# Optimization experiments

Hardware: AMD Instinct MI355X
Metric: run time of the kernel (lower is better)

## Reference

```python
import jax, jax.numpy as jnp
import numpy as np

NU, NM, E, L = 100000, 20000, 3200000, 1000000
FD, H = 128, 64


def setup_inputs() -> dict:
    key = jax.random.key(0)
    ks = jax.random.split(key, 32)
    s = 0.05
    inp = {
        'movie_x': jax.random.normal(ks[0], (NM, FD), jnp.float32),
        'edge_src_user': jax.random.randint(ks[1], (E,), 0, NU),
        'edge_dst_movie': jax.random.randint(ks[2], (E,), 0, NM),
        'label_user': jax.random.randint(ks[3], (L,), 0, NU),
        'label_movie': jax.random.randint(ks[4], (L,), 0, NM),
        'user_emb': jax.random.normal(ks[5], (NU, H), jnp.float32) * s,
        'proj_w': jax.random.normal(ks[6], (FD, H), jnp.float32) * s,
        'proj_b': jnp.zeros((H,), jnp.float32),
        'dec_w1': jax.random.normal(ks[7], (2 * H, H), jnp.float32) * s,
        'dec_b1': jnp.zeros((H,), jnp.float32),
        'dec_w2': jax.random.normal(ks[8], (H, 1), jnp.float32) * s,
        'dec_b2': jnp.zeros((1,), jnp.float32),
    }
    i = 9
    for layer in ('1', '2'):
        for rel in ('um', 'mu'):
            inp[f'w{layer}_{rel}_l'] = jax.random.normal(ks[i], (H, H), jnp.float32) * s; i += 1
            inp[f'b{layer}_{rel}_l'] = jnp.zeros((H,), jnp.float32)
            inp[f'w{layer}_{rel}_r'] = jax.random.normal(ks[i], (H, H), jnp.float32) * s; i += 1
    return inp


def _sage(x_src, x_dst, e_src, e_dst, n_dst, w_l, b_l, w_r):
    # PyG SAGEConv, aggr='mean': out = lin_l(mean_j x_src[j]) + lin_r(x_dst)
    msg = x_src[e_src]                                      # [E, H] gather
    agg = jax.ops.segment_sum(msg, e_dst, num_segments=n_dst)
    cnt = jax.ops.segment_sum(jnp.ones((e_dst.shape[0],), x_src.dtype), e_dst, num_segments=n_dst)
    agg = agg / jnp.maximum(cnt, 1.0)[:, None]
    return agg @ w_l + b_l + x_dst @ w_r


def reference(movie_x, edge_src_user, edge_dst_movie, label_user, label_movie,
              user_emb, proj_w, proj_b,
              w1_um_l, b1_um_l, w1_um_r, w1_mu_l, b1_mu_l, w1_mu_r,
              w2_um_l, b2_um_l, w2_um_r, w2_mu_l, b2_mu_l, w2_mu_r,
              dec_w1, dec_b1, dec_w2, dec_b2):
    nu, nm = user_emb.shape[0], movie_x.shape[0]
    user0 = user_emb
    movie0 = movie_x @ proj_w + proj_b
    # conv1 (user->movie and movie->user), then ReLU
    movie1 = jax.nn.relu(_sage(user0, movie0, edge_src_user, edge_dst_movie, nm, w1_um_l, b1_um_l, w1_um_r))
    user1 = jax.nn.relu(_sage(movie0, user0, edge_dst_movie, edge_src_user, nu, w1_mu_l, b1_mu_l, w1_mu_r))
    # conv2 (no activation)
    movie2 = _sage(user1, movie1, edge_src_user, edge_dst_movie, nm, w2_um_l, b2_um_l, w2_um_r)
    user2 = _sage(movie1, user1, edge_dst_movie, edge_src_user, nu, w2_mu_l, b2_mu_l, w2_mu_r)
    # edge decoder: gather -> concat -> MLP
    x = jnp.concatenate([user2[label_user], movie2[label_movie]], axis=-1)  # [L, 2H]
    x = jax.nn.relu(x @ dec_w1 + dec_b1)
    return x @ dec_w2 + dec_b2
```

## Files before the change

### kernel.cpp

```cpp
#include <hip/hip_runtime.h>

static constexpr int NU = 100000;
static constexpr int NM = 20000;
static constexpr int NE = 3200000;
static constexpr int NL = 1000000;
static constexpr int FD = 128;
static constexpr int H  = 64;

static constexpr int MBK = 16;
static constexpr int UBK = 64;
static constexpr int NBM = NM / MBK;
static constexpr int NBU = (NU + UBK - 1) / UBK;
static constexpr int CAP_M = 4096;
static constexpr int CAP_U = 3072;
static constexpr int B3C = 16384;

typedef __attribute__((ext_vector_type(8))) short short8v;
typedef __attribute__((ext_vector_type(4))) float f32x4;

__device__ __forceinline__ ushort bf16rne(float x) {
  unsigned u = __float_as_uint(x);
  return (ushort)((u + 0x7fffu + ((u >> 16) & 1u)) >> 16);
}

__global__ void k_binit2(int* __restrict__ bcur_m, int* __restrict__ bcur_u) {
  int i = blockIdx.x * 256 + threadIdx.x;
  if (i < NBM) bcur_m[i] = i * CAP_M;
  if (i < NBU) bcur_u[i] = i * CAP_U;
}

__global__ void __launch_bounds__(256) k_bin3(
    const int* __restrict__ esrc, const int* __restrict__ edst,
    int* __restrict__ bcur_m, int* __restrict__ bcur_u,
    unsigned* __restrict__ pairs_m, unsigned* __restrict__ pairs_u, int nbPerSide) {
  __shared__ int cnt[NBU];
  __shared__ int base[NBU];
  int tid = threadIdx.x;
  bool um = (int)blockIdx.x < nbPerSide;
  int cb = um ? blockIdx.x : blockIdx.x - nbPerSide;
  int nbs = um ? NBM : NBU;
  int sh = um ? 4 : 6;
  int* bcur = um ? bcur_m : bcur_u;
  unsigned* pairs = um ? pairs_m : pairs_u;
  const int* keys = um ? edst : esrc;
  const int* vals = um ? esrc : edst;
  int e0 = cb * B3C, e1 = min(e0 + B3C, NE);
  for (int i = tid; i < nbs; i += 256) cnt[i] = 0;
  __syncthreads();
  for (int e = e0 + (tid << 2); e < e1; e += 1024) {
    int4 k = *(const int4*)(keys + e);
    atomicAdd(&cnt[k.x >> sh], 1);
    atomicAdd(&cnt[k.y >> sh], 1);
    atomicAdd(&cnt[k.z >> sh], 1);
    atomicAdd(&cnt[k.w >> sh], 1);
  }
  __syncthreads();
  for (int i = tid; i < nbs; i += 256) {
    int c = cnt[i];
    if (c > 0) base[i] = atomicAdd(&bcur[i], c);
    cnt[i] = 0;
  }
  __syncthreads();
  int lsh = um ? 17 : 15;
  unsigned lmask = um ? 15u : 63u;
  for (int e = e0 + (tid << 2); e < e1; e += 1024) {
    int4 k = *(const int4*)(keys + e);
    int4 v = *(const int4*)(vals + e);
    int ks[4] = {k.x, k.y, k.z, k.w};
    int vs[4] = {v.x, v.y, v.z, v.w};
    #pragma unroll
    for (int j = 0; j < 4; ++j) {
      int b = ks[j] >> sh;
      int r = atomicAdd(&cnt[b], 1);
      pairs[base[b] + r] = (((unsigned)ks[j] & lmask) << lsh) | (unsigned)vs[j];
    }
  }
}

__global__ void __launch_bounds__(256) k_sortb4(
    const unsigned* __restrict__ pairs_m, const unsigned* __restrict__ pairs_u,
    const int* __restrict__ bcur_m, const int* __restrict__ bcur_u,
    int* __restrict__ st_m, int* __restrict__ dg_m, int* __restrict__ out_m,
    int* __restrict__ st_u, int* __restrict__ dg_u, ushort* __restrict__ out_u) {
  __shared__ int cnt[64];
  __shared__ int cbase[64];
  const unsigned* pairs; const int* bcur; int* start; int* deg;
  int b, npb, shift, cap, n; unsigned mask;
  bool um = (int)blockIdx.x < NBM;
  if (um) {
    pairs = pairs_m; bcur = bcur_m; start = st_m; deg = dg_m;
    b = blockIdx.x; npb = MBK; shift = 17; mask = 0x1FFFFu; cap = CAP_M; n = NM;
  } else {
    pairs = pairs_u; bcur = bcur_u; start = st_u; deg = dg_u;
    b = blockIdx.x - NBM; npb = UBK; shift = 15; mask = 0x7FFFu; cap = CAP_U; n = NU;
  }
  int tid = threadIdx.x;
  if (tid < 64) cnt[tid] = 0;
  __syncthreads();
  int e0 = b * cap, e1 = bcur[b];
  for (int e = e0 + tid; e < e1; e += 256) atomicAdd(&cnt[pairs[e] >> shift], 1);
  __syncthreads();
  if (tid < 64) {
    int c = cnt[tid];
    int v = c;
    #pragma unroll
    for (int off = 1; off < 64; off <<= 1) {
      int t = __shfl_up(v, off, 64);
      if (tid >= off) v += t;
    }
    int basee = e0 + v - c;
    cbase[tid] = basee;
    int node = b * npb + tid;
    if (tid < npb && node < n) { start[node] = basee; deg[node] = c; }
    cnt[tid] = 0;
  }
  __syncthreads();
  for (int e = e0 + tid; e < e1; e += 256) {
    unsigned v = pairs[e];
    int loc = (int)(v >> shift);
    int r = atomicAdd(&cnt[loc], 1);
    if (um) out_m[cbase[loc] + r] = (int)(v & mask);
    else    out_u[cbase[loc] + r] = (ushort)(v & mask);
  }
}

#define ACC4(vv)                                                           \
  a0 += __uint_as_float((vv).x << 16); a1 += __uint_as_float((vv).x & 0xffff0000u); \
  a2 += __uint_as_float((vv).y << 16); a3 += __uint_as_float((vv).y & 0xffff0000u); \
  a4 += __uint_as_float((vv).z << 16); a5 += __uint_as_float((vv).z & 0xffff0000u); \
  a6 += __uint_as_float((vv).w << 16); a7 += __uint_as_float((vv).w & 0xffff0000u);

__device__ __forceinline__ void agg_node_w8(const ushort* __restrict__ feat,
                                            const int* __restrict__ idxs,
                                            int s, int degn, float* __restrict__ out,
                                            int d, int lane) {
  int f8 = lane & 7, p = lane >> 3;
  int e = s + degn;
  float a0 = 0.f, a1 = 0.f, a2 = 0.f, a3 = 0.f, a4 = 0.f, a5 = 0.f, a6 = 0.f, a7 = 0.f;
  int i = s;
  for (; i + 32 <= e; i += 32) {
    int s0 = idxs[i + 0 + p];
    int s1 = idxs[i + 8 + p];
    int s2 = idxs[i + 16 + p];
    int s3 = idxs[i + 24 + p];
    uint4 v0 = *(const uint4*)(feat + ((size_t)s0 << 6) + (f8 << 3));
    uint4 v1 = *(const uint4*)(feat + ((size_t)s1 << 6) + (f8 << 3));
    uint4 v2 = *(const uint4*)(feat + ((size_t)s2 << 6) + (f8 << 3));
    uint4 v3 = *(const uint4*)(feat + ((size_t)s3 << 6) + (f8 << 3));
    ACC4(v0) ACC4(v1) ACC4(v2) ACC4(v3)
  }
  for (; i < e; i += 8) {
    int ii = i + p;
    bool ok = ii < e;
    int sj = idxs[ok ? ii : i];
    uint4 v = *(const uint4*)(feat + ((size_t)sj << 6) + (f8 << 3));
    if (!ok) { v.x = 0u; v.y = 0u; v.z = 0u; v.w = 0u; }
    ACC4(v)
  }
  #pragma unroll
  for (int m = 8; m < 64; m <<= 1) {
    a0 += __shfl_xor(a0, m, 64); a1 += __shfl_xor(a1, m, 64);
    a2 += __shfl_xor(a2, m, 64); a3 += __shfl_xor(a3, m, 64);
    a4 += __shfl_xor(a4, m, 64); a5 += __shfl_xor(a5, m, 64);
    a6 += __shfl_xor(a6, m, 64); a7 += __shfl_xor(a7, m, 64);
  }
  if (p == 0) {
    float inv = 1.f / fmaxf((float)degn, 1.f);
    float4 o0 = make_float4(a0 * inv, a1 * inv, a2 * inv, a3 * inv);
    float4 o1 = make_float4(a4 * inv, a5 * inv, a6 * inv, a7 * inv);
    *(float4*)&out[((size_t)d << 6) + (f8 << 3)] = o0;
    *(float4*)&out[((size_t)d << 6) + (f8 << 3) + 4] = o1;
  }
}

__device__ __forceinline__ void agg_node_w4(const ushort* __restrict__ feat,
                                            const ushort* __restrict__ idxs,
                                            int s, int degn, float* __restrict__ out,
                                            int d, int lane) {
  int f4 = lane & 15, p = lane >> 4;
  int e = s + degn;
  float a0 = 0.f, a1 = 0.f, a2 = 0.f, a3 = 0.f;
  int i = s;
  for (; i + 16 <= e; i += 16) {
    int s0 = idxs[i + 0 + p];
    int s1 = idxs[i + 4 + p];
    int s2 = idxs[i + 8 + p];
    int s3 = idxs[i + 12 + p];
    uint2 v0 = *(const uint2*)(feat + ((size_t)s0 << 6) + (f4 << 2));
    uint2 v1 = *(const uint2*)(feat + ((size_t)s1 << 6) + (f4 << 2));
    uint2 v2 = *(const uint2*)(feat + ((size_t)s2 << 6) + (f4 << 2));
    uint2 v3 = *(const uint2*)(feat + ((size_t)s3 << 6) + (f4 << 2));
    a0 += __uint_as_float(v0.x << 16); a1 += __uint_as_float(v0.x & 0xffff0000u);
    a2 += __uint_as_float(v0.y << 16); a3 += __uint_as_float(v0.y & 0xffff0000u);
    a0 += __uint_as_float(v1.x << 16); a1 += __uint_as_float(v1.x & 0xffff0000u);
    a2 += __uint_as_float(v1.y << 16); a3 += __uint_as_float(v1.y & 0xffff0000u);
    a0 += __uint_as_float(v2.x << 16); a1 += __uint_as_float(v2.x & 0xffff0000u);
    a2 += __uint_as_float(v2.y << 16); a3 += __uint_as_float(v2.y & 0xffff0000u);
    a0 += __uint_as_float(v3.x << 16); a1 += __uint_as_float(v3.x & 0xffff0000u);
    a2 += __uint_as_float(v3.y << 16); a3 += __uint_as_float(v3.y & 0xffff0000u);
  }
  for (; i < e; i += 4) {
    int ii = i + p;
    bool ok = ii < e;
    int sj = idxs[ok ? ii : i];
    uint2 v = *(const uint2*)(feat + ((size_t)sj << 6) + (f4 << 2));
    if (!ok) { v.x = 0u; v.y = 0u; }
    a0 += __uint_as_float(v.x << 16); a1 += __uint_as_float(v.x & 0xffff0000u);
    a2 += __uint_as_float(v.y << 16); a3 += __uint_as_float(v.y & 0xffff0000u);
  }
  a0 += __shfl_xor(a0, 16, 64); a1 += __shfl_xor(a1, 16, 64);
  a2 += __shfl_xor(a2, 16, 64); a3 += __shfl_xor(a3, 16, 64);
  a0 += __shfl_xor(a0, 32, 64); a1 += __shfl_xor(a1, 32, 64);
  a2 += __shfl_xor(a2, 32, 64); a3 += __shfl_xor(a3, 32, 64);
  if (p == 0) {
    float inv = 1.f / fmaxf((float)degn, 1.f);
    float4 o = make_float4(a0 * inv, a1 * inv, a2 * inv, a3 * inv);
    *(float4*)&out[((size_t)d << 6) + (f4 << 2)] = o;
  }
}

__global__ void __launch_bounds__(256) k_agg2d(
    int gm,
    const ushort* __restrict__ fM, const int* __restrict__ stM, const int* __restrict__ dgM,
    const int* __restrict__ idxM, float* __restrict__ outM, int nM,
    const ushort* __restrict__ fU, const int* __restrict__ stU, const int* __restrict__ dgU,
    const ushort* __restrict__ idxU, float* __restrict__ outU, int nU) {
  int lane = threadIdx.x & 63;
  if ((int)blockIdx.x < gm) {
    int d = blockIdx.x * 4 + (threadIdx.x >> 6);
    if (d >= nM) return;
    agg_node_w8(fM, idxM, stM[d], dgM[d], outM, d, lane);
  } else {
    int d = (blockIdx.x - gm) * 4 + (threadIdx.x >> 6);
    if (d >= nU) return;
    agg_node_w4(fU, idxU, stU[d], dgU[d], outU, d, lane);
  }
}

__global__ void __launch_bounds__(256) k_proj16(const float* __restrict__ x,
                                                const float* __restrict__ w,
                                                const float* __restrict__ b,
                                                float* __restrict__ out,
                                                ushort* __restrict__ outh) {
  __shared__ float sw[FD * H];
  __shared__ float sx[16][FD];
  int tid = threadIdx.x;
  int r0 = blockIdx.x * 16;
  #pragma unroll
  for (int it = 0; it < 8; ++it) {
    int idx = tid + it * 256;
    ((float4*)sw)[idx] = ((const float4*)w)[idx];
  }
  #pragma unroll
  for (int it = 0; it < 2; ++it) {
    int idx = tid + it * 256;
    int row = idx >> 5, q = idx & 31;
    *(float4*)&sx[row][q * 4] = ((const float4*)x)[(size_t)(r0 + row) * 32 + q];
  }
  __syncthreads();
  int col = tid & 63, rg = tid >> 6;
  float bb = b[col];
  float acc[4];
  #pragma unroll
  for (int j = 0; j < 4; ++j) acc[j] = bb;
  #pragma unroll 4
  for (int k4 = 0; k4 < 32; ++k4) {
    float w0 = sw[(k4 * 4 + 0) * H + col], w1 = sw[(k4 * 4 + 1) * H + col];
    float w2 = sw[(k4 * 4 + 2) * H + col], w3 = sw[(k4 * 4 + 3) * H + col];
    #pragma unroll
    for (int j = 0; j < 4; ++j) {
      float4 a = *(const float4*)&sx[rg + j * 4][k4 * 4];
      acc[j] += a.x * w0 + a.y * w1 + a.z * w2 + a.w * w3;
    }
  }
  #pragma unroll
  for (int j = 0; j < 4; ++j) {
    size_t o = (size_t)(r0 + rg + j * 4) * H + col;
    out[o] = acc[j];
    outh[o] = bf16rne(acc[j]);
  }
}

__global__ void __launch_bounds__(256) k_sage16(
    int gm,
    const float* __restrict__ aggM, const float* __restrict__ xdM,
    const float* __restrict__ wlM, const float* __restrict__ wrM,
    const float* __restrict__ blM, float* __restrict__ outfM, ushort* __restrict__ outhM,
    const float* __restrict__ aggU, const float* __restrict__ xdU,
    const float* __restrict__ wlU, const float* __restrict__ wrU,
    const float* __restrict__ blU, float* __restrict__ outfU, ushort* __restrict__ outhU,
    int relu) {
  __shared__ float swl[H * H];
  __shared__ float swr[H * H];
  __shared__ float sa[16][H];
  __shared__ float sd[16][H];
  int tid = threadIdx.x;
  const float *agg, *xd, *wl, *wr, *bl; float* outf; ushort* outh; int r0;
  if ((int)blockIdx.x < gm) {
    agg = aggM; xd = xdM; wl = wlM; wr = wrM; bl = blM; outf = outfM; outh = outhM;
    r0 = blockIdx.x * 16;
  } else {
    agg = aggU; xd = xdU; wl = wlU; wr = wrU; bl = blU; outf = outfU; outh = outhU;
    r0 = (blockIdx.x - gm) * 16;
  }
  #pragma unroll
  for (int it = 0; it < 4; ++it) {
    int idx = tid + it * 256;
    ((float4*)swl)[idx] = ((const float4*)wl)[idx];
    ((float4*)swr)[idx] = ((const float4*)wr)[idx];
  }
  {
    int row = tid >> 4, q = tid & 15;
    *(float4*)&sa[row][q * 4] = ((const float4*)agg)[(size_t)(r0 + row) * 16 + q];
    *(float4*)&sd[row][q * 4] = ((const float4*)xd)[(size_t)(r0 + row) * 16 + q];
  }
  __syncthreads();
  int col = tid & 63, rg = tid >> 6;
  float b = bl[col];
  float acc[4];
  #pragma unroll
  for (int j = 0; j < 4; ++j) acc[j] = b;
  #pragma unroll 4
  for (int k4 = 0; k4 < 16; ++k4) {
    float w0 = swl[(k4 * 4 + 0) * H + col], w1 = swl[(k4 * 4 + 1) * H + col];
    float w2 = swl[(k4 * 4 + 2) * H + col], w3 = swl[(k4 * 4 + 3) * H + col];
    float v0 = swr[(k4 * 4 + 0) * H + col], v1 = swr[(k4 * 4 + 1) * H + col];
    float v2 = swr[(k4 * 4 + 2) * H + col], v3 = swr[(k4 * 4 + 3) * H + col];
    #pragma unroll
    for (int j = 0; j < 4; ++j) {
      int r = rg + j * 4;
      float4 a = *(const float4*)&sa[r][k4 * 4];
      float4 d = *(const float4*)&sd[r][k4 * 4];
      acc[j] += a.x * w0 + a.y * w1 + a.z * w2 + a.w * w3;
      acc[j] += d.x * v0 + d.y * v1 + d.z * v2 + d.w * v3;
    }
  }
  #pragma unroll
  for (int j = 0; j < 4; ++j) {
    int r = rg + j * 4;
    float v = relu ? fmaxf(acc[j], 0.f) : acc[j];
    size_t o = (size_t)(r0 + r) * H + col;
    if (outf) outf[o] = v;
    if (outh) outh[o] = bf16rne(v);
  }
}

__global__ void __launch_bounds__(256) k_cvtb(const float* __restrict__ src,
                                              ushort* __restrict__ dst, int n4) {
  int i = blockIdx.x * 256 + threadIdx.x;
  if (i >= n4) return;
  float4 v = ((const float4*)src)[i];
  ushort4 o;
  o.x = bf16rne(v.x); o.y = bf16rne(v.y); o.z = bf16rne(v.z); o.w = bf16rne(v.w);
  ((ushort4*)dst)[i] = o;
}

__global__ void k_packw(const float* __restrict__ w1, ushort* __restrict__ pw) {
  int tid = threadIdx.x;
  for (int it = 0; it < 4; ++it) {
    int q = tid + it * 256;
    int kt = q >> 8, ct = (q >> 6) & 3, l = q & 63;
    int kg = l >> 4, cg = l & 15;
    #pragma unroll
    for (int j = 0; j < 8; ++j) {
      int k = kt * 32 + kg * 8 + j;
      int c = ct * 16 + cg;
      float x = w1[k * 64 + c];
      unsigned u = __float_as_uint(x);
      unsigned r = (u + 0x7fffu + ((u >> 16) & 1u)) >> 16;
      float res = x - __uint_as_float(r << 16);
      pw[q * 8 + j] = (ushort)r;
      pw[8192 + q * 8 + j] = (ushort)(__float_as_uint(res) >> 16);
    }
  }
}

__global__ void __launch_bounds__(256) k_dec_mfma(
    const ushort* __restrict__ uhi, const ushort* __restrict__ mhi,
    const int* __restrict__ lu, const int* __restrict__ lm,
    const ushort* __restrict__ pw,
    const float* __restrict__ b1, const float* __restrict__ w2,
    const float* __restrict__ b2, float* __restrict__ out) {
  __shared__ ushort sB[2 * 16 * 64 * 8];
  int tid = threadIdx.x;
  #pragma unroll
  for (int it = 0; it < 8; ++it) {
    int idx = tid + it * 256;
    ((float4*)sB)[idx] = ((const float4*)pw)[idx];
  }
  __syncthreads();
  int l = tid & 63, w = tid >> 6;
  int cg = l & 15, kg = l >> 4;
  float w2f[4], b1f[4];
  #pragma unroll
  for (int ct = 0; ct < 4; ++ct) {
    w2f[ct] = w2[ct * 16 + cg];
    b1f[ct] = b1[ct * 16 + cg];
  }
  float b2v = b2[0];
  for (int t = 0; t < 4; ++t) {
    int Lb = blockIdx.x * 256 + w * 64 + t * 16;
    int lab = min(Lb + cg, NL - 1);
    int nu = lu[lab], nm = lm[lab];
    const size_t ub = (size_t)nu * 64 + kg * 8;
    const size_t mb = (size_t)nm * 64 + kg * 8;
    short8v ah[4];
    ah[0] = *(const short8v*)(uhi + ub);
    ah[1] = *(const short8v*)(uhi + ub + 32);
    ah[2] = *(const short8v*)(mhi + mb);
    ah[3] = *(const short8v*)(mhi + mb + 32);
    f32x4 acc[4];
    #pragma unroll
    for (int ct = 0; ct < 4; ++ct) acc[ct] = (f32x4){b1f[ct], b1f[ct], b1f[ct], b1f[ct]};
    #pragma unroll
    for (int kt = 0; kt < 4; ++kt) {
      #pragma unroll
      for (int ct = 0; ct < 4; ++ct) {
        const int f = kt * 4 + ct;
        short8v bh = *(const short8v*)&sB[(size_t)(f * 64 + l) * 8];
        short8v bl_ = *(const short8v*)&sB[(size_t)((16 + f) * 64 + l) * 8];
        acc[ct] = __builtin_amdgcn_mfma_f32_16x16x32_bf16(ah[kt], bh, acc[ct], 0, 0, 0);
        acc[ct] = __builtin_amdgcn_mfma_f32_16x16x32_bf16(ah[kt], bl_, acc[ct], 0, 0, 0);
      }
    }
    float p[4];
    #pragma unroll
    for (int r = 0; r < 4; ++r) {
      p[r] = fmaxf(acc[0][r], 0.f) * w2f[0] + fmaxf(acc[1][r], 0.f) * w2f[1] +
             fmaxf(acc[2][r], 0.f) * w2f[2] + fmaxf(acc[3][r], 0.f) * w2f[3];
    }
    #pragma unroll
    for (int m = 8; m >= 1; m >>= 1) {
      #pragma unroll
      for (int r = 0; r < 4; ++r) p[r] += __shfl_xor(p[r], m, 64);
    }
    if (cg == 0) {
      #pragma unroll
      for (int r = 0; r < 4; ++r) {
        int row = Lb + kg * 4 + r;
        if (row < NL) out[row] = p[r] + b2v;
      }
    }
  }
}

extern "C" void kernel_launch(void* const* d_in, const int* in_sizes, int n_in,
                              void* d_out, int out_size, void* d_ws, size_t ws_size,
                              hipStream_t stream) {
  const float* movie_x  = (const float*)d_in[0];
  const int*   esrc     = (const int*)d_in[1];
  const int*   edst     = (const int*)d_in[2];
  const int*   lu       = (const int*)d_in[3];
  const int*   lm       = (const int*)d_in[4];
  const float* user_emb = (const float*)d_in[5];
  const float* proj_w   = (const float*)d_in[6];
  const float* proj_b   = (const float*)d_in[7];
  const float* dec_w1   = (const float*)d_in[8];
  const float* dec_b1   = (const float*)d_in[9];
  const float* dec_w2   = (const float*)d_in[10];
  const float* dec_b2   = (const float*)d_in[11];
  const float* w1_um_l  = (const float*)d_in[12];
  const float* b1_um_l  = (const float*)d_in[13];
  const float* w1_um_r  = (const float*)d_in[14];
  const float* w1_mu_l  = (const float*)d_in[15];
  const float* b1_mu_l  = (const float*)d_in[16];
  const float* w1_mu_r  = (const float*)d_in[17];
  const float* w2_um_l  = (const float*)d_in[18];
  const float* b2_um_l  = (const float*)d_in[19];
  const float* w2_um_r  = (const float*)d_in[20];
  const float* w2_mu_l  = (const float*)d_in[21];
  const float* b2_mu_l  = (const float*)d_in[22];
  const float* w2_mu_r  = (const float*)d_in[23];

  char* ws = (char*)d_ws;
  size_t off = 0;
  auto alloc = [&](size_t bytes) {
    void* p = ws + off;
    off = (off + bytes + 255) & ~(size_t)255;
    return p;
  };
  float* movie0   = (float*)alloc((size_t)NM * H * 4);
  float* movie1   = (float*)alloc((size_t)NM * H * 4);
  float* user1    = (float*)alloc((size_t)NU * H * 4);
  float* agg_m    = (float*)alloc((size_t)NM * H * 4);
  float* agg_u    = (float*)alloc((size_t)NU * H * 4);
  unsigned* pairs_m = (unsigned*)user1;
  unsigned* pairs_u = pairs_m + (size_t)NBM * CAP_M;
  ushort* uembh   = (ushort*)alloc((size_t)NU * H * 2);
  ushort* movie0h = (ushort*)alloc((size_t)NM * H * 2);
  ushort* movie1h = (ushort*)alloc((size_t)NM * H * 2);
  ushort* user1h  = (ushort*)alloc((size_t)NU * H * 2);
  ushort* uhi     = (ushort*)alloc((size_t)NU * H * 2);
  ushort* mhi     = (ushort*)alloc((size_t)NM * H * 2);
  int* st_m      = (int*)alloc((size_t)NM * 4);
  int* st_u      = (int*)alloc((size_t)NU * 4);
  int* dg_m      = (int*)alloc((size_t)NM * 4);
  int* dg_u      = (int*)alloc((size_t)NU * 4);
  int* bcur_m    = (int*)alloc((size_t)NBM * 4);
  int* bcur_u    = (int*)alloc((size_t)NBU * 4);
  int* su_by_m   = (int*)alloc((size_t)NBM * CAP_M * 4);
  ushort* sm_by_u = (ushort*)alloc((size_t)NBU * CAP_U * 2);
  ushort* pw     = (ushort*)alloc((size_t)2 * 16 * 64 * 8 * 2);
  (void)ws_size; (void)in_sizes; (void)n_in; (void)out_size;

  k_binit2<<<(NBU + 255) / 256, 256, 0, stream>>>(bcur_m, bcur_u);
  int nbPerSide = (NE + B3C - 1) / B3C;
  k_bin3<<<2 * nbPerSide, 256, 0, stream>>>(esrc, edst, bcur_m, bcur_u,
                                            pairs_m, pairs_u, nbPerSide);
  k_sortb4<<<NBM + NBU, 256, 0, stream>>>(pairs_m, pairs_u, bcur_m, bcur_u,
                                          st_m, dg_m, su_by_m, st_u, dg_u, sm_by_u);

  k_proj16<<<NM / 16, 256, 0, stream>>>(movie_x, proj_w, proj_b, movie0, movie0h);
  k_cvtb<<<(NU * H / 4 + 255) / 256, 256, 0, stream>>>(user_emb, uembh, NU * H / 4);
  k_packw<<<1, 256, 0, stream>>>(dec_w1, pw);

  const int GAM = NM / 4, GAU = NU / 4;
  const int GSM = NM / 16, GSU = NU / 16;

  k_agg2d<<<GAM + GAU, 256, 0, stream>>>(GAM,
      uembh,   st_m, dg_m, su_by_m, agg_m, NM,
      movie0h, st_u, dg_u, sm_by_u, agg_u, NU);
  k_sage16<<<GSM + GSU, 256, 0, stream>>>(GSM,
      agg_m, movie0,   w1_um_l, w1_um_r, b1_um_l, movie1, movie1h,
      agg_u, user_emb, w1_mu_l, w1_mu_r, b1_mu_l, user1,  user1h, 1);

  k_agg2d<<<GAM + GAU, 256, 0, stream>>>(GAM,
      user1h,  st_m, dg_m, su_by_m, agg_m, NM,
      movie1h, st_u, dg_u, sm_by_u, agg_u, NU);
  k_sage16<<<GSM + GSU, 256, 0, stream>>>(GSM,
      agg_m, movie1, w2_um_l, w2_um_r, b2_um_l, (float*)nullptr, mhi,
      agg_u, user1,  w2_mu_l, w2_mu_r, b2_mu_l, (float*)nullptr, uhi, 0);

  k_dec_mfma<<<(NL + 255) / 256, 256, 0, stream>>>(uhi, mhi, lu, lm, pw,
                                                   dec_b1, dec_w2, dec_b2, (float*)d_out);
}
```

Before: 485.8 us.

## Unify aggregation path, fuse prep kernels, and double sage tile rows

Four separate changes are bundled. The aggregation loop becomes one template with a compile-time gather unroll, and the user-side aggregation switches from 4-wide to 8-wide lanes with 16-byte loads. The projection, user-embedding bf16 conversion and decoder weight packing are merged into one launch to cut launch overhead. The sage kernel now handles 32 rows per block instead of 16, reusing the staged weights over more rows at the cost of more registers and shared memory.

```diff
diff --git a/kernel.cpp b/kernel.cpp
--- a/kernel.cpp
+++ b/kernel.cpp
@@ -130,29 +130,29 @@
   a4 += __uint_as_float((vv).z << 16); a5 += __uint_as_float((vv).z & 0xffff0000u); \
   a6 += __uint_as_float((vv).w << 16); a7 += __uint_as_float((vv).w & 0xffff0000u);
 
+template <typename IdxT, int UN>
 __device__ __forceinline__ void agg_node_w8(const ushort* __restrict__ feat,
-                                            const int* __restrict__ idxs,
+                                            const IdxT* __restrict__ idxs,
                                             int s, int degn, float* __restrict__ out,
                                             int d, int lane) {
   int f8 = lane & 7, p = lane >> 3;
   int e = s + degn;
   float a0 = 0.f, a1 = 0.f, a2 = 0.f, a3 = 0.f, a4 = 0.f, a5 = 0.f, a6 = 0.f, a7 = 0.f;
   int i = s;
-  for (; i + 32 <= e; i += 32) {
-    int s0 = idxs[i + 0 + p];
-    int s1 = idxs[i + 8 + p];
-    int s2 = idxs[i + 16 + p];
-    int s3 = idxs[i + 24 + p];
-    uint4 v0 = *(const uint4*)(feat + ((size_t)s0 << 6) + (f8 << 3));
-    uint4 v1 = *(const uint4*)(feat + ((size_t)s1 << 6) + (f8 << 3));
-    uint4 v2 = *(const uint4*)(feat + ((size_t)s2 << 6) + (f8 << 3));
-    uint4 v3 = *(const uint4*)(feat + ((size_t)s3 << 6) + (f8 << 3));
-    ACC4(v0) ACC4(v1) ACC4(v2) ACC4(v3)
+  for (; i + 8 * UN <= e; i += 8 * UN) {
+    uint4 v[UN];
+    #pragma unroll
+    for (int k = 0; k < UN; ++k) {
+      int sj = (int)idxs[i + 8 * k + p];
+      v[k] = *(const uint4*)(feat + ((size_t)sj << 6) + (f8 << 3));
+    }
+    #pragma unroll
+    for (int k = 0; k < UN; ++k) { ACC4(v[k]) }
   }
   for (; i < e; i += 8) {
     int ii = i + p;
     bool ok = ii < e;
-    int sj = idxs[ok ? ii : i];
+    int sj = (int)idxs[ok ? ii : i];
     uint4 v = *(const uint4*)(feat + ((size_t)sj << 6) + (f8 << 3));
     if (!ok) { v.x = 0u; v.y = 0u; v.z = 0u; v.w = 0u; }
     ACC4(v)
@@ -173,53 +173,7 @@
   }
 }
 
-__device__ __forceinline__ void agg_node_w4(const ushort* __restrict__ feat,
-                                            const ushort* __restrict__ idxs,
-                                            int s, int degn, float* __restrict__ out,
-                                            int d, int lane) {
-  int f4 = lane & 15, p = lane >> 4;
-  int e = s + degn;
-  float a0 = 0.f, a1 = 0.f, a2 = 0.f, a3 = 0.f;
-  int i = s;
-  for (; i + 16 <= e; i += 16) {
-    int s0 = idxs[i + 0 + p];
-    int s1 = idxs[i + 4 + p];
-    int s2 = idxs[i + 8 + p];
-    int s3 = idxs[i + 12 + p];
-    uint2 v0 = *(const uint2*)(feat + ((size_t)s0 << 6) + (f4 << 2));
-    uint2 v1 = *(const uint2*)(feat + ((size_t)s1 << 6) + (f4 << 2));
-    uint2 v2 = *(const uint2*)(feat + ((size_t)s2 << 6) + (f4 << 2));
-    uint2 v3 = *(const uint2*)(feat + ((size_t)s3 << 6) + (f4 << 2));
-    a0 += __uint_as_float(v0.x << 16); a1 += __uint_as_float(v0.x & 0xffff0000u);
-    a2 += __uint_as_float(v0.y << 16); a3 += __uint_as_float(v0.y & 0xffff0000u);
-    a0 += __uint_as_float(v1.x << 16); a1 += __uint_as_float(v1.x & 0xffff0000u);
-    a2 += __uint_as_float(v1.y << 16); a3 += __uint_as_float(v1.y & 0xffff0000u);
-    a0 += __uint_as_float(v2.x << 16); a1 += __uint_as_float(v2.x & 0xffff0000u);
-    a2 += __uint_as_float(v2.y << 16); a3 += __uint_as_float(v2.y & 0xffff0000u);
-    a0 += __uint_as_float(v3.x << 16); a1 += __uint_as_float(v3.x & 0xffff0000u);
-    a2 += __uint_as_float(v3.y << 16); a3 += __uint_as_float(v3.y & 0xffff0000u);
-  }
-  for (; i < e; i += 4) {
-    int ii = i + p;
-    bool ok = ii < e;
-    int sj = idxs[ok ? ii : i];
-    uint2 v = *(const uint2*)(feat + ((size_t)sj << 6) + (f4 << 2));
-    if (!ok) { v.x = 0u; v.y = 0u; }
-    a0 += __uint_as_float(v.x << 16); a1 += __uint_as_float(v.x & 0xffff0000u);
-    a2 += __uint_as_float(v.y << 16); a3 += __uint_as_float(v.y & 0xffff0000u);
-  }
-  a0 += __shfl_xor(a0, 16, 64); a1 += __shfl_xor(a1, 16, 64);
-  a2 += __shfl_xor(a2, 16, 64); a3 += __shfl_xor(a3, 16, 64);
-  a0 += __shfl_xor(a0, 32, 64); a1 += __shfl_xor(a1, 32, 64);
-  a2 += __shfl_xor(a2, 32, 64); a3 += __shfl_xor(a3, 32, 64);
-  if (p == 0) {
-    float inv = 1.f / fmaxf((float)degn, 1.f);
-    float4 o = make_float4(a0 * inv, a1 * inv, a2 * inv, a3 * inv);
-    *(float4*)&out[((size_t)d << 6) + (f4 << 2)] = o;
-  }
-}
-
-__global__ void __launch_bounds__(256) k_agg2d(
+__global__ void __launch_bounds__(256) k_agg2e(
     int gm,
     const ushort* __restrict__ fM, const int* __restrict__ stM, const int* __restrict__ dgM,
     const int* __restrict__ idxM, float* __restrict__ outM, int nM,
@@ -229,59 +183,87 @@
   if ((int)blockIdx.x < gm) {
     int d = blockIdx.x * 4 + (threadIdx.x >> 6);
     if (d >= nM) return;
-    agg_node_w8(fM, idxM, stM[d], dgM[d], outM, d, lane);
+    agg_node_w8<int, 8>(fM, idxM, stM[d], dgM[d], outM, d, lane);
   } else {
     int d = (blockIdx.x - gm) * 4 + (threadIdx.x >> 6);
     if (d >= nU) return;
-    agg_node_w4(fU, idxU, stU[d], dgU[d], outU, d, lane);
-  }
-}
-
-__global__ void __launch_bounds__(256) k_proj16(const float* __restrict__ x,
-                                                const float* __restrict__ w,
-                                                const float* __restrict__ b,
-                                                float* __restrict__ out,
-                                                ushort* __restrict__ outh) {
+    agg_node_w8<ushort, 4>(fU, idxU, stU[d], dgU[d], outU, d, lane);
+  }
+}
+
+static constexpr int PB = NM / 16;
+static constexpr int CB = (NU * H / 4) / 256;
+__global__ void __launch_bounds__(256) k_prep(
+    const float* __restrict__ x, const float* __restrict__ w, const float* __restrict__ b,
+    float* __restrict__ out, ushort* __restrict__ outh,
+    const float* __restrict__ uemb, ushort* __restrict__ uembh,
+    const float* __restrict__ w1, ushort* __restrict__ pw) {
   __shared__ float sw[FD * H];
   __shared__ float sx[16][FD];
   int tid = threadIdx.x;
-  int r0 = blockIdx.x * 16;
-  #pragma unroll
-  for (int it = 0; it < 8; ++it) {
-    int idx = tid + it * 256;
-    ((float4*)sw)[idx] = ((const float4*)w)[idx];
-  }
-  #pragma unroll
-  for (int it = 0; it < 2; ++it) {
-    int idx = tid + it * 256;
-    int row = idx >> 5, q = idx & 31;
-    *(float4*)&sx[row][q * 4] = ((const float4*)x)[(size_t)(r0 + row) * 32 + q];
-  }
-  __syncthreads();
-  int col = tid & 63, rg = tid >> 6;
-  float bb = b[col];
-  float acc[4];
-  #pragma unroll
-  for (int j = 0; j < 4; ++j) acc[j] = bb;
-  #pragma unroll 4
-  for (int k4 = 0; k4 < 32; ++k4) {
-    float w0 = sw[(k4 * 4 + 0) * H + col], w1 = sw[(k4 * 4 + 1) * H + col];
-    float w2 = sw[(k4 * 4 + 2) * H + col], w3 = sw[(k4 * 4 + 3) * H + col];
+  int blk = blockIdx.x;
+  if (blk < PB) {
+    int r0 = blk * 16;
+    #pragma unroll
+    for (int it = 0; it < 8; ++it) {
+      int idx = tid + it * 256;
+      ((float4*)sw)[idx] = ((const float4*)w)[idx];
+    }
+    #pragma unroll
+    for (int it = 0; it < 2; ++it) {
+      int idx = tid + it * 256;
+      int row = idx >> 5, q = idx & 31;
+      *(float4*)&sx[row][q * 4] = ((const float4*)x)[(size_t)(r0 + row) * 32 + q];
+    }
+    __syncthreads();
+    int col = tid & 63, rg = tid >> 6;
+    float bb = b[col];
+    float acc[4];
+    #pragma unroll
+    for (int j = 0; j < 4; ++j) acc[j] = bb;
+    #pragma unroll 4
+    for (int k4 = 0; k4 < 32; ++k4) {
+      float w0 = sw[(k4 * 4 + 0) * H + col], w1_ = sw[(k4 * 4 + 1) * H + col];
+      float w2 = sw[(k4 * 4 + 2) * H + col], w3 = sw[(k4 * 4 + 3) * H + col];
+      #pragma unroll
+      for (int j = 0; j < 4; ++j) {
+        float4 a = *(const float4*)&sx[rg + j * 4][k4 * 4];
+        acc[j] += a.x * w0 + a.y * w1_ + a.z * w2 + a.w * w3;
+      }
+    }
     #pragma unroll
     for (int j = 0; j < 4; ++j) {
-      float4 a = *(const float4*)&sx[rg + j * 4][k4 * 4];
-      acc[j] += a.x * w0 + a.y * w1 + a.z * w2 + a.w * w3;
-    }
-  }
-  #pragma unroll
-  for (int j = 0; j < 4; ++j) {
-    size_t o = (size_t)(r0 + rg + j * 4) * H + col;
-    out[o] = acc[j];
-    outh[o] = bf16rne(acc[j]);
-  }
-}
-
-__global__ void __launch_bounds__(256) k_sage16(
+      size_t o = (size_t)(r0 + rg + j * 4) * H + col;
+      out[o] = acc[j];
+      outh[o] = bf16rne(acc[j]);
+    }
+  } else if (blk < PB + CB) {
+    int i = (blk - PB) * 256 + tid;
+    float4 v = ((const float4*)uemb)[i];
+    ushort4 o;
+    o.x = bf16rne(v.x); o.y = bf16rne(v.y); o.z = bf16rne(v.z); o.w = bf16rne(v.w);
+    ((ushort4*)uembh)[i] = o;
+  } else {
+    for (int it = 0; it < 4; ++it) {
+      int q = tid + it * 256;
+      int kt = q >> 8, ct = (q >> 6) & 3, l = q & 63;
+      int kg = l >> 4, cg = l & 15;
+      #pragma unroll
+      for (int j = 0; j < 8; ++j) {
+        int k = kt * 32 + kg * 8 + j;
+        int c = ct * 16 + cg;
+        float xv = w1[k * 64 + c];
+        unsigned u = __float_as_uint(xv);
+        unsigned r = (u + 0x7fffu + ((u >> 16) & 1u)) >> 16;
+        float res = xv - __uint_as_float(r << 16);
+        pw[q * 8 + j] = (ushort)r;
+        pw[8192 + q * 8 + j] = (ushort)(__float_as_uint(res) >> 16);
+      }
+    }
+  }
+}
+
+__global__ void __launch_bounds__(256) k_sage32(
     int gm,
     const float* __restrict__ aggM, const float* __restrict__ xdM,
     const float* __restrict__ wlM, const float* __restrict__ wrM,
@@ -292,16 +274,16 @@
     int relu) {
   __shared__ float swl[H * H];
   __shared__ float swr[H * H];
-  __shared__ float sa[16][H];
-  __shared__ float sd[16][H];
+  __shared__ float sa[32][H];
+  __shared__ float sd[32][H];
   int tid = threadIdx.x;
   const float *agg, *xd, *wl, *wr, *bl; float* outf; ushort* outh; int r0;
   if ((int)blockIdx.x < gm) {
     agg = aggM; xd = xdM; wl = wlM; wr = wrM; bl = blM; outf = outfM; outh = outhM;
-    r0 = blockIdx.x * 16;
+    r0 = blockIdx.x * 32;
   } else {
     agg = aggU; xd = xdU; wl = wlU; wr = wrU; bl = blU; outf = outfU; outh = outhU;
-    r0 = (blockIdx.x - gm) * 16;
+    r0 = (blockIdx.x - gm) * 32;
   }
   #pragma unroll
   for (int it = 0; it < 4; ++it) {
@@ -309,25 +291,27 @@
     ((float4*)swl)[idx] = ((const float4*)wl)[idx];
     ((float4*)swr)[idx] = ((const float4*)wr)[idx];
   }
-  {
-    int row = tid >> 4, q = tid & 15;
+  #pragma unroll
+  for (int it = 0; it < 2; ++it) {
+    int idx = tid + it * 256;
+    int row = idx >> 4, q = idx & 15;
     *(float4*)&sa[row][q * 4] = ((const float4*)agg)[(size_t)(r0 + row) * 16 + q];
     *(float4*)&sd[row][q * 4] = ((const float4*)xd)[(size_t)(r0 + row) * 16 + q];
   }
   __syncthreads();
   int col = tid & 63, rg = tid >> 6;
   float b = bl[col];
-  float acc[4];
-  #pragma unroll
-  for (int j = 0; j < 4; ++j) acc[j] = b;
-  #pragma unroll 4
+  float acc[8];
+  #pragma unroll
+  for (int j = 0; j < 8; ++j) acc[j] = b;
+  #pragma unroll 2
   for (int k4 = 0; k4 < 16; ++k4) {
     float w0 = swl[(k4 * 4 + 0) * H + col], w1 = swl[(k4 * 4 + 1) * H + col];
     float w2 = swl[(k4 * 4 + 2) * H + col], w3 = swl[(k4 * 4 + 3) * H + col];
     float v0 = swr[(k4 * 4 + 0) * H + col], v1 = swr[(k4 * 4 + 1) * H + col];
     float v2 = swr[(k4 * 4 + 2) * H + col], v3 = swr[(k4 * 4 + 3) * H + col];
     #pragma unroll
-    for (int j = 0; j < 4; ++j) {
+    for (int j = 0; j < 8; ++j) {
       int r = rg + j * 4;
       float4 a = *(const float4*)&sa[r][k4 * 4];
       float4 d = *(const float4*)&sd[r][k4 * 4];
@@ -336,42 +320,12 @@
     }
   }
   #pragma unroll
-  for (int j = 0; j < 4; ++j) {
+  for (int j = 0; j < 8; ++j) {
     int r = rg + j * 4;
     float v = relu ? fmaxf(acc[j], 0.f) : acc[j];
     size_t o = (size_t)(r0 + r) * H + col;
     if (outf) outf[o] = v;
     if (outh) outh[o] = bf16rne(v);
-  }
-}
-
-__global__ void __launch_bounds__(256) k_cvtb(const float* __restrict__ src,
-                                              ushort* __restrict__ dst, int n4) {
-  int i = blockIdx.x * 256 + threadIdx.x;
-  if (i >= n4) return;
-  float4 v = ((const float4*)src)[i];
-  ushort4 o;
-  o.x = bf16rne(v.x); o.y = bf16rne(v.y); o.z = bf16rne(v.z); o.w = bf16rne(v.w);
-  ((ushort4*)dst)[i] = o;
-}
-
-__global__ void k_packw(const float* __restrict__ w1, ushort* __restrict__ pw) {
-  int tid = threadIdx.x;
-  for (int it = 0; it < 4; ++it) {
-    int q = tid + it * 256;
-    int kt = q >> 8, ct = (q >> 6) & 3, l = q & 63;
-    int kg = l >> 4, cg = l & 15;
-    #pragma unroll
-    for (int j = 0; j < 8; ++j) {
-      int k = kt * 32 + kg * 8 + j;
-      int c = ct * 16 + cg;
-      float x = w1[k * 64 + c];
-      unsigned u = __float_as_uint(x);
-      unsigned r = (u + 0x7fffu + ((u >> 16) & 1u)) >> 16;
-      float res = x - __uint_as_float(r << 16);
-      pw[q * 8 + j] = (ushort)r;
-      pw[8192 + q * 8 + j] = (ushort)(__float_as_uint(res) >> 16);
-    }
   }
 }
 
@@ -510,24 +464,23 @@
   k_sortb4<<<NBM + NBU, 256, 0, stream>>>(pairs_m, pairs_u, bcur_m, bcur_u,
                                           st_m, dg_m, su_by_m, st_u, dg_u, sm_by_u);
 
-  k_proj16<<<NM / 16, 256, 0, stream>>>(movie_x, proj_w, proj_b, movie0, movie0h);
-  k_cvtb<<<(NU * H / 4 + 255) / 256, 256, 0, stream>>>(user_emb, uembh, NU * H / 4);
-  k_packw<<<1, 256, 0, stream>>>(dec_w1, pw);
+  k_prep<<<PB + CB + 1, 256, 0, stream>>>(movie_x, proj_w, proj_b, movie0, movie0h,
+                                          user_emb, uembh, dec_w1, pw);
 
   const int GAM = NM / 4, GAU = NU / 4;
-  const int GSM = NM / 16, GSU = NU / 16;
-
-  k_agg2d<<<GAM + GAU, 256, 0, stream>>>(GAM,
+  const int GSM = NM / 32, GSU = NU / 32;
+
+  k_agg2e<<<GAM + GAU, 256, 0, stream>>>(GAM,
       uembh,   st_m, dg_m, su_by_m, agg_m, NM,
       movie0h, st_u, dg_u, sm_by_u, agg_u, NU);
-  k_sage16<<<GSM + GSU, 256, 0, stream>>>(GSM,
+  k_sage32<<<GSM + GSU, 256, 0, stream>>>(GSM,
       agg_m, movie0,   w1_um_l, w1_um_r, b1_um_l, movie1, movie1h,
       agg_u, user_emb, w1_mu_l, w1_mu_r, b1_mu_l, user1,  user1h, 1);
 
-  k_agg2d<<<GAM + GAU, 256, 0, stream>>>(GAM,
+  k_agg2e<<<GAM + GAU, 256, 0, stream>>>(GAM,
       user1h,  st_m, dg_m, su_by_m, agg_m, NM,
       movie1h, st_u, dg_u, sm_by_u, agg_u, NU);
-  k_sage16<<<GSM + GSU, 256, 0, stream>>>(GSM,
+  k_sage32<<<GSM + GSU, 256, 0, stream>>>(GSM,
       agg_m, movie1, w2_um_l, w2_um_r, b2_um_l, (float*)nullptr, mhi,
       agg_u, user1,  w2_mu_l, w2_mu_r, b2_mu_l, (float*)nullptr, uhi, 0);
 
```

Result: slower. 496.7 us (+2.2%).
